# Kernel tuning notes

Hardware: AMD Instinct MI355X
Metric: run time of the kernel (lower is better)

Reference implementation:

```python
import jax, jax.numpy as jnp
import numpy as np
from jax import lax

# ---- model dims ----
NTOKEN = 60697
D_MODEL = 512
NLAYERS = 4
D_STATE = 16
D_CONV = 4
EXPAND = 2
D_INNER = EXPAND * D_MODEL      # 1024
DT_RANK = (D_MODEL + 15) // 16  # 32 (ceil(d_model/16), mamba default)
B_SZ = 4
SEQ = 2048
EPS = 1e-5


def setup_inputs() -> dict:
    key = jax.random.key(0)
    ks = jax.random.split(key, 16)
    s = 0.02
    src = jax.random.randint(ks[0], (B_SZ, SEQ), 0, NTOKEN)
    src_key_padding_mask = jnp.ones((B_SZ, SEQ), dtype=bool)
    emb_w = jax.random.normal(ks[1], (NTOKEN, D_MODEL), jnp.float32) * s
    enc_ln_w = jnp.ones((D_MODEL,), jnp.float32)
    enc_ln_b = jnp.zeros((D_MODEL,), jnp.float32)
    ln_w = jnp.ones((NLAYERS, D_MODEL), jnp.float32)
    ln_b = jnp.zeros((NLAYERS, D_MODEL), jnp.float32)
    in_proj_w = jax.random.normal(ks[2], (NLAYERS, 2 * D_INNER, D_MODEL), jnp.float32) * s
    conv_w = jax.random.normal(ks[3], (NLAYERS, D_INNER, D_CONV), jnp.float32) * 0.1
    conv_b = jnp.zeros((NLAYERS, D_INNER), jnp.float32)
    x_proj_w = jax.random.normal(ks[4], (NLAYERS, DT_RANK + 2 * D_STATE, D_INNER), jnp.float32) * s
    dt_proj_w = jax.random.normal(ks[5], (NLAYERS, D_INNER, DT_RANK), jnp.float32) * (DT_RANK ** -0.5)
    dt_proj_b = jax.random.uniform(ks[6], (NLAYERS, D_INNER), jnp.float32, -4.0, -2.0)
    # S4D real init: A = -[1..d_state], stored as log
    A_log = jnp.log(jnp.broadcast_to(jnp.arange(1, D_STATE + 1, dtype=jnp.float32),
                                     (NLAYERS, D_INNER, D_STATE)))
    D_skip = jnp.ones((NLAYERS, D_INNER), jnp.float32)
    out_proj_w = jax.random.normal(ks[7], (NLAYERS, D_MODEL, D_INNER), jnp.float32) * s / np.sqrt(NLAYERS)
    normf_w = jnp.ones((D_MODEL,), jnp.float32)
    normf_b = jnp.zeros((D_MODEL,), jnp.float32)
    return {
        'src': src, 'src_key_padding_mask': src_key_padding_mask,
        'emb_w': emb_w, 'enc_ln_w': enc_ln_w, 'enc_ln_b': enc_ln_b,
        'ln_w': ln_w, 'ln_b': ln_b, 'in_proj_w': in_proj_w,
        'conv_w': conv_w, 'conv_b': conv_b, 'x_proj_w': x_proj_w,
        'dt_proj_w': dt_proj_w, 'dt_proj_b': dt_proj_b,
        'A_log': A_log, 'D_skip': D_skip, 'out_proj_w': out_proj_w,
        'normf_w': normf_w, 'normf_b': normf_b,
    }


def _layer_norm(x, w, b, eps=EPS):
    mu = jnp.mean(x, axis=-1, keepdims=True)
    var = jnp.mean(jnp.square(x - mu), axis=-1, keepdims=True)
    return (x - mu) * lax.rsqrt(var + eps) * w + b


def _mamba_mixer(h, in_w, cw, cb, xw, dtw, dtb, A_log, D_skip, ow):
    B, L, _ = h.shape
    xz = h @ in_w.T                                   # [B,L,2*d_inner]
    x, z = jnp.split(xz, 2, axis=-1)
    # causal depthwise conv1d, kernel D_CONV
    xt = x.swapaxes(1, 2)                             # [B,d_inner,L]
    xp = jnp.pad(xt, ((0, 0), (0, 0), (D_CONV - 1, 0)))
    conv = cb[None, :, None]
    for k in range(D_CONV):
        conv = conv + cw[:, k][None, :, None] * xp[:, :, k:k + L]
    x = jax.nn.silu(conv).swapaxes(1, 2)              # [B,L,d_inner]
    xdbl = x @ xw.T                                   # [B,L,dt_rank+2*d_state]
    dt = jax.nn.softplus(xdbl[..., :DT_RANK] @ dtw.T + dtb)      # [B,L,d_inner]
    Bm = xdbl[..., DT_RANK:DT_RANK + D_STATE]                    # [B,L,d_state]
    Cm = xdbl[..., DT_RANK + D_STATE:]                           # [B,L,d_state]
    A = -jnp.exp(A_log)                               # [d_inner,d_state]

    def step(hst, inp):
        dt_t, b_t, c_t, x_t = inp                     # [B,d_inner],[B,d_state],[B,d_state],[B,d_inner]
        dA = jnp.exp(dt_t[..., None] * A)             # [B,d_inner,d_state]
        hst = dA * hst + (dt_t * x_t)[..., None] * b_t[:, None, :]
        y_t = jnp.einsum('bds,bs->bd', hst, c_t)
        return hst, y_t

    xs = (dt.swapaxes(0, 1), Bm.swapaxes(0, 1), Cm.swapaxes(0, 1), x.swapaxes(0, 1))
    h0 = jnp.zeros((B, D_INNER, D_STATE), dtype=h.dtype)
    _, ys = lax.scan(step, h0, xs)                    # ys: [L,B,d_inner]
    y = ys.swapaxes(0, 1) + x * D_skip
    y = y * jax.nn.silu(z)
    return y @ ow.T


def reference(src, src_key_padding_mask, emb_w, enc_ln_w, enc_ln_b, ln_w, ln_b,
              in_proj_w, conv_w, conv_b, x_proj_w, dt_proj_w, dt_proj_b,
              A_log, D_skip, out_proj_w, normf_w, normf_b):
    # GeneEncoder: embedding -> LayerNorm (dropout = identity in eval)
    hidden = _layer_norm(emb_w[src], enc_ln_w, enc_ln_b)
    residual = None
    for i in range(NLAYERS):  # prenorm Mamba Blocks
        residual = hidden if residual is None else hidden + residual
        hidden = _mamba_mixer(_layer_norm(residual, ln_w[i], ln_b[i]),
                              in_proj_w[i], conv_w[i], conv_b[i], x_proj_w[i],
                              dt_proj_w[i], dt_proj_b[i], A_log[i], D_skip[i],
                              out_proj_w[i])
    residual = hidden + residual
    return _layer_norm(residual, normf_w, normf_b)
```

## Files before the change

### kernel.cpp

```cpp
#include <hip/hip_runtime.h>
#include <hip/hip_bf16.h>
#include <math.h>

#define NTOKEN 60697
#define D_MODEL 512
#define NLAYERS 4
#define D_STATE 16
#define D_CONV 4
#define D_INNER 1024
#define DT_RANK 32
#define B_SZ 4
#define SEQ 2048
#define EPS 1e-5f
#define NROWS (B_SZ * SEQ)
#define CHUNK 128
#define NCHUNK (SEQ / CHUNK)

typedef __bf16 bf16_t;
typedef __attribute__((ext_vector_type(8))) __bf16 bfx8;
typedef __attribute__((ext_vector_type(4))) __bf16 bfx4;
typedef __attribute__((ext_vector_type(4))) float f32x4;


__device__ __forceinline__ float fast_sigmoid(float x) {
    return 1.0f / (1.0f + __expf(-x));
}
__device__ __forceinline__ float silu(float x) {
    return x * fast_sigmoid(x);
}
__device__ __forceinline__ float softplus_f(float x) {
    return (x > 20.0f) ? x : log1pf(__expf(x));
}

__device__ __forceinline__ void gload_lds16(const void* g, void* l) {
    __builtin_amdgcn_global_load_lds(
        (const __attribute__((address_space(1))) unsigned int*)g,
        (__attribute__((address_space(3))) unsigned int*)l, 16, 0, 0);
}

template <int CTRL>
__device__ __forceinline__ float dpp_fetch(float x) {
    int xi = __builtin_bit_cast(int, x);
    int yi = __builtin_amdgcn_update_dpp(0, xi, CTRL, 0xF, 0xF, true);
    return __builtin_bit_cast(float, yi);
}
__device__ __forceinline__ float dpp_sum16(float p) {
    p += dpp_fetch<0xB1>(p);
    p += dpp_fetch<0x4E>(p);
    p += dpp_fetch<0x141>(p);
    p += dpp_fetch<0x140>(p);
    return p;
}

__device__ __forceinline__ float blk_reduce_sum(float x, float* sbuf) {
#pragma unroll
    for (int m = 32; m >= 1; m >>= 1) x += __shfl_xor(x, m);
    int wid = threadIdx.x >> 6;
    if ((threadIdx.x & 63) == 0) sbuf[wid] = x;
    __syncthreads();
    float t = sbuf[0] + sbuf[1] + sbuf[2] + sbuf[3];
    __syncthreads();
    return t;
}

__global__ __launch_bounds__(256) void cast_bf16_kernel(
    const float* __restrict__ in, bf16_t* __restrict__ out, size_t n)
{
    size_t stride = (size_t)gridDim.x * 256 * 4;
    for (size_t i = ((size_t)blockIdx.x * 256 + threadIdx.x) * 4; i < n; i += stride) {
        float4 v = *reinterpret_cast<const float4*>(in + i);
        bfx4 o;
        o[0] = (bf16_t)v.x; o[1] = (bf16_t)v.y;
        o[2] = (bf16_t)v.z; o[3] = (bf16_t)v.w;
        *reinterpret_cast<bfx4*>(out + i) = o;
    }
}

__global__ __launch_bounds__(256) void weff_kernel(
    const float* __restrict__ dtw, const float* __restrict__ xw,
    bf16_t* __restrict__ Weff)
{
    int L = blockIdx.y;
    int idx = blockIdx.x * 256 + threadIdx.x;
    int n = idx >> 10, k = idx & 1023;
    const float* dtwL = dtw + (size_t)L * D_INNER * DT_RANK;
    const float* xwL  = xw  + (size_t)L * (DT_RANK + 2 * D_STATE) * D_INNER;
    float acc = 0.f;
#pragma unroll
    for (int r = 0; r < DT_RANK; r++)
        acc += dtwL[n * DT_RANK + r] * xwL[r * D_INNER + k];
    Weff[(size_t)L * D_INNER * D_INNER + idx] = (bf16_t)acc;
}


__global__ __launch_bounds__(256) void embed_ln_kernel(
    const int* __restrict__ src, const float* __restrict__ emb,
    const float* __restrict__ w, const float* __restrict__ b,
    float* __restrict__ R)
{
    __shared__ float sbuf[4];
    int row = blockIdx.x;
    int tok = src[row];
    const float* e = emb + (size_t)tok * D_MODEL;
    int c0 = threadIdx.x, c1 = threadIdx.x + 256;
    float v0 = e[c0], v1 = e[c1];
    float mu = blk_reduce_sum(v0 + v1, sbuf) * (1.0f / D_MODEL);
    float d0 = v0 - mu, d1 = v1 - mu;
    float var = blk_reduce_sum(d0 * d0 + d1 * d1, sbuf) * (1.0f / D_MODEL);
    float rs = rsqrtf(var + EPS);
    size_t base = (size_t)row * D_MODEL;
    R[base + c0] = d0 * rs * w[c0] + b[c0];
    R[base + c1] = d1 * rs * w[c1] + b[c1];
}

__global__ __launch_bounds__(256) void add_ln_kernel(
    float* __restrict__ R, const float* __restrict__ Hadd,
    const float* __restrict__ w, const float* __restrict__ b,
    float* __restrict__ out, bf16_t* __restrict__ outb)
{
    __shared__ float sbuf[4];
    size_t base = (size_t)blockIdx.x * D_MODEL;
    int c0 = threadIdx.x, c1 = c0 + 256;
    float v0 = R[base + c0], v1 = R[base + c1];
    if (Hadd) {
        v0 += Hadd[base + c0];
        v1 += Hadd[base + c1];
        R[base + c0] = v0;
        R[base + c1] = v1;
    }
    float mu = blk_reduce_sum(v0 + v1, sbuf) * (1.0f / D_MODEL);
    float d0 = v0 - mu, d1 = v1 - mu;
    float var = blk_reduce_sum(d0 * d0 + d1 * d1, sbuf) * (1.0f / D_MODEL);
    float rs = rsqrtf(var + EPS);
    float o0 = d0 * rs * w[c0] + b[c0];
    float o1 = d1 * rs * w[c1] + b[c1];
    if (out) {
        out[base + c0] = o0;
        out[base + c1] = o1;
    }
    if (outb) {
        outb[base + c0] = (bf16_t)o0;
        outb[base + c1] = (bf16_t)o1;
    }
}

template <int EPI>
__global__ __launch_bounds__(256) void gemm_bf16_nt(
    const bf16_t* __restrict__ A, const bf16_t* __restrict__ B,
    float* __restrict__ C, int ldc, int K, const float* __restrict__ bias,
    const unsigned short* __restrict__ xcb_u16,
    unsigned short* __restrict__ dtx_u16,
    float* __restrict__ Cz)
{
    __shared__ bf16_t As[128 * 32];
    __shared__ bf16_t Bs[128 * 32];
    int tid = threadIdx.x;
    int lane = tid & 63, wid = tid >> 6;
    int m0 = blockIdx.y * 128, n0 = blockIdx.x * 128;
    int wm = (wid >> 1) * 64, wn = (wid & 1) * 64;
    int c_lo = lane & 15;
    int khalf = lane >> 4;

    f32x4 acc[4][4];
#pragma unroll
    for (int i = 0; i < 4; i++)
#pragma unroll
        for (int j = 0; j < 4; j++)
            acc[i][j] = (f32x4){0.f, 0.f, 0.f, 0.f};

    for (int k0 = 0; k0 < K; k0 += 32) {
#pragma unroll
        for (int i = 0; i < 2; i++) {
            int c = i * 256 + tid;
            int row = c >> 2;
            int cb = (c & 3) * 16;
            int ldsoff = (i * 256 + wid * 64) * 16;
            gload_lds16((const char*)A + ((size_t)(m0 + row) * K + k0) * 2 + cb,
                        (char*)As + ldsoff);
            gload_lds16((const char*)B + ((size_t)(n0 + row) * K + k0) * 2 + cb,
                        (char*)Bs + ldsoff);
        }
        __syncthreads();

        bfx8 af[4], bfr[4];
#pragma unroll
        for (int i = 0; i < 4; i++) {
            af[i]  = *reinterpret_cast<const bfx8*>(As + (wm + i * 16 + c_lo) * 32 + khalf * 8);
            bfr[i] = *reinterpret_cast<const bfx8*>(Bs + (wn + i * 16 + c_lo) * 32 + khalf * 8);
        }
#pragma unroll
        for (int i = 0; i < 4; i++)
#pragma unroll
            for (int j = 0; j < 4; j++)
                acc[i][j] = __builtin_amdgcn_mfma_f32_16x16x32_bf16(af[i], bfr[j], acc[i][j], 0, 0, 0);
        __syncthreads();
    }

#pragma unroll
    for (int i = 0; i < 4; i++) {
#pragma unroll
        for (int j = 0; j < 4; j++) {
            int row0 = m0 + wm + i * 16 + khalf * 4;
            int col = n0 + wn + j * 16 + c_lo;
#pragma unroll
            for (int r = 0; r < 4; r++) {
                int row = row0 + r;
                float v = acc[i][j][r];
                if (EPI == 0) {
                    C[(size_t)row * ldc + col] = v;
                } else if (EPI == 2) {
                    v = softplus_f(v + bias[col]);
                    unsigned int db = (unsigned int)__builtin_bit_cast(unsigned short, (bf16_t)v);
                    unsigned int xb = (unsigned int)xcb_u16[(size_t)row * D_INNER + col];
                    *(unsigned int*)(dtx_u16 + (size_t)row * 2048 + 2 * col) = db | (xb << 16);
                } else if (EPI == 3) {
                    if (col < D_INNER) C[(size_t)row * D_INNER + col] = v;
                    else               Cz[(size_t)row * D_INNER + col - D_INNER] = v;
                }
            }
        }
    }
}

__global__ __launch_bounds__(128) void gemm_bc_bf16(
    const bf16_t* __restrict__ A, const bf16_t* __restrict__ Bmat,
    float* __restrict__ BCX, int K)
{
    __shared__ bf16_t As[64 * 32];
    __shared__ bf16_t Bs[32 * 32];
    int tid = threadIdx.x;
    int lane = tid & 63, w = tid >> 6;
    int m0 = blockIdx.x * 64;
    int wr0 = w * 32;
    int c_lo = lane & 15;
    int khalf = lane >> 4;

    f32x4 acc[2][2];
#pragma unroll
    for (int i = 0; i < 2; i++)
#pragma unroll
        for (int j = 0; j < 2; j++)
            acc[i][j] = (f32x4){0.f, 0.f, 0.f, 0.f};

    for (int k0 = 0; k0 < K; k0 += 32) {
        {
            int c = tid;
            gload_lds16((const char*)A + ((size_t)(m0 + (c >> 2)) * K + k0) * 2 + (c & 3) * 16,
                        (char*)As + w * 1024);
        }
        {
            int c = tid + 128;
            gload_lds16((const char*)A + ((size_t)(m0 + (c >> 2)) * K + k0) * 2 + (c & 3) * 16,
                        (char*)As + 2048 + w * 1024);
        }
        {
            int c = tid;
            gload_lds16((const char*)Bmat + ((size_t)(c >> 2) * K + k0) * 2 + (c & 3) * 16,
                        (char*)Bs + w * 1024);
        }
        __syncthreads();

        bfx8 af[2], bfr[2];
#pragma unroll
        for (int i = 0; i < 2; i++)
            af[i] = *reinterpret_cast<const bfx8*>(As + (wr0 + i * 16 + c_lo) * 32 + khalf * 8);
#pragma unroll
        for (int j = 0; j < 2; j++)
            bfr[j] = *reinterpret_cast<const bfx8*>(Bs + (j * 16 + c_lo) * 32 + khalf * 8);
#pragma unroll
        for (int i = 0; i < 2; i++)
#pragma unroll
            for (int j = 0; j < 2; j++)
                acc[i][j] = __builtin_amdgcn_mfma_f32_16x16x32_bf16(af[i], bfr[j], acc[i][j], 0, 0, 0);
        __syncthreads();
    }

#pragma unroll
    for (int i = 0; i < 2; i++)
#pragma unroll
        for (int j = 0; j < 2; j++) {
            int row0 = m0 + wr0 + i * 16 + khalf * 4;
#pragma unroll
            for (int r = 0; r < 4; r++)
                BCX[(size_t)(row0 + r) * 32 + 2 * c_lo + j] = acc[i][j][r];
        }
}

__global__ __launch_bounds__(256) void conv_silu_kernel(
    const float* __restrict__ Xraw, const float* __restrict__ cw,
    const float* __restrict__ cb, bf16_t* __restrict__ XCb)
{
    size_t gid = (size_t)blockIdx.x * 256 + threadIdx.x;
    int d = (int)(gid & (D_INNER - 1));
    size_t bt = gid >> 10;
    int t = (int)(bt & (SEQ - 1));
    float acc = cb[d];
#pragma unroll
    for (int k = 0; k < D_CONV; k++) {
        int tt = t + k - (D_CONV - 1);
        if (tt >= 0)
            acc += cw[d * D_CONV + k] * Xraw[(bt + (size_t)(k - (D_CONV - 1))) * D_INNER + d];
    }
    XCb[gid] = (bf16_t)silu(acc);
}

__device__ __forceinline__ void scan_stage(
    char* base, const unsigned int* __restrict__ DTXb,
    const float* __restrict__ BCX, size_t r0, int d0, int w, int lane)
{
    if (w < 2) {
        int cdt = w * 64 + lane;
        gload_lds16((const char*)DTXb + ((r0 + (cdt >> 2)) * 1024 + d0) * 4 + (cdt & 3) * 16,
                    base + w * 1024);
        int cbc = 128 + w * 64;
        gload_lds16((const char*)BCX + (r0 + ((cbc + lane) >> 3)) * 128 + ((cbc + lane) & 7) * 16,
                    base + 2048 + cbc * 16);
    } else {
        int cbc = (w - 2) * 64;
        gload_lds16((const char*)BCX + (r0 + ((cbc + lane) >> 3)) * 128 + ((cbc + lane) & 7) * 16,
                    base + 2048 + cbc * 16);
    }
}

__global__ __launch_bounds__(256) void scan_pA_kernel(
    const unsigned int* __restrict__ DTXb, const float* __restrict__ BCX,
    const float* __restrict__ A_log,
    float* __restrict__ DcB, float* __restrict__ UcB)
{
    __shared__ __align__(16) char lds[2][6144];
    const int tid = threadIdx.x;
    const int w = tid >> 6, lane = tid & 63;
    const int s = tid & 15, dl = tid >> 4;
    const int b = blockIdx.x >> 6;
    const int d0 = (blockIdx.x & 63) * 16;
    const int c = blockIdx.y;
    const int d = d0 + dl;
    const float Av = -__expf(A_log[d * D_STATE + s]);
    const size_t bbase = (size_t)b * SEQ;
    const int tstart = c * CHUNK;

    float h = 0.f, cum = 0.f;
    scan_stage(lds[0], DTXb, BCX, bbase + tstart, d0, w, lane);
    __syncthreads();
    int cur = 0;
    for (int t0 = 0; t0 < CHUNK; t0 += 32) {
        if (t0 + 32 < CHUNK)
            scan_stage(lds[cur ^ 1], DTXb, BCX, bbase + tstart + t0 + 32, d0, w, lane);
        const char* L = lds[cur];
#pragma unroll
        for (int kk = 0; kk < 32; kk++) {
            unsigned int pk = *(const unsigned int*)(L + kk * 64 + dl * 4);
            float dtv = __builtin_bit_cast(float, pk << 16);
            float xv  = __builtin_bit_cast(float, pk & 0xFFFF0000u);
            float bv  = *(const float*)(L + 2048 + kk * 128 + s * 8);
            float e = __expf(dtv * Av);
            h = fmaf(e, h, dtv * xv * bv);
            cum += dtv;
        }
        __syncthreads();
        cur ^= 1;
    }
    size_t cb64 = ((size_t)c * B_SZ + b) * D_INNER + d;
    UcB[cb64 * 16 + s] = h;
    if (s == 0) DcB[cb64] = cum;
}

__global__ __launch_bounds__(256) void scan_p2_kernel(
    const float* __restrict__ A_log, const float* __restrict__ DcB,
    const float* __restrict__ UcB, float* __restrict__ HcB)
{
    int tid = threadIdx.x;
    int s = tid & 15, dl = tid >> 4;
    int chain = blockIdx.x * 16 + dl;
    int b = chain >> 10, d = chain & 1023;
    float Av = -__expf(A_log[d * D_STATE + s]);
    float Hv = 0.f;
    for (int c = 0; c < NCHUNK; c++) {
        size_t base = ((size_t)c * B_SZ + b) * D_INNER + d;
        HcB[base * 16 + s] = Hv;
        Hv = __expf(Av * DcB[base]) * Hv + UcB[base * 16 + s];
    }
}

__global__ __launch_bounds__(256) void scan_pB_kernel(
    const unsigned int* __restrict__ DTXb, const float* __restrict__ BCX,
    const float* __restrict__ HcB, const float* __restrict__ A_log,
    const float* __restrict__ Zbuf, const float* __restrict__ Dskip,
    bf16_t* __restrict__ XCb)
{
    __shared__ __align__(16) char lds[2][6144];
    __shared__ float ytile[32][17];
    const int tid = threadIdx.x;
    const int w = tid >> 6, lane = tid & 63;
    const int s = tid & 15, dl = tid >> 4;
    const int b = blockIdx.x >> 6;
    const int d0 = (blockIdx.x & 63) * 16;
    const int c = blockIdx.y;
    const int d = d0 + dl;
    const float Av = -__expf(A_log[d * D_STATE + s]);
    const size_t bbase = (size_t)b * SEQ;
    const int tstart = c * CHUNK;

    float h = HcB[(((size_t)c * B_SZ + b) * D_INNER + d) * 16 + s];

    const int tl  = tid >> 3;
    const int dlo = (tid * 2) & 15;
    const float dsk0 = Dskip[d0 + dlo];
    const float dsk1 = Dskip[d0 + dlo + 1];

    scan_stage(lds[0], DTXb, BCX, bbase + tstart, d0, w, lane);
    __syncthreads();
    int cur = 0;
    for (int t0 = 0; t0 < CHUNK; t0 += 32) {
        if (t0 + 32 < CHUNK)
            scan_stage(lds[cur ^ 1], DTXb, BCX, bbase + tstart + t0 + 32, d0, w, lane);
        const char* L = lds[cur];
#pragma unroll
        for (int half = 0; half < 2; half++) {
            float yhold = 0.f;
#pragma unroll
            for (int k = 0; k < 16; k++) {
                int kk = half * 16 + k;
                unsigned int pk = *(const unsigned int*)(L + kk * 64 + dl * 4);
                float dtv = __builtin_bit_cast(float, pk << 16);
                float xv  = __builtin_bit_cast(float, pk & 0xFFFF0000u);
                float2 bc = *(const float2*)(L + 2048 + kk * 128 + s * 8);
                float e = __expf(dtv * Av);
                h = fmaf(e, h, dtv * xv * bc.x);
                float p = dpp_sum16(h * bc.y);
                if (s == k) yhold = p;
            }
            ytile[half * 16 + s][dl] = yhold;
        }
        __syncthreads();

        {
            int t = tstart + t0 + tl;
            size_t row = (bbase + t) * (size_t)D_INNER + d0 + dlo;
            float y0 = ytile[tl][dlo];
            float y1 = ytile[tl][dlo + 1];
            unsigned int xw = *(const unsigned int*)(XCb + row);
            float x0 = __builtin_bit_cast(float, xw << 16);
            float x1 = __builtin_bit_cast(float, xw & 0xFFFF0000u);
            float2 z2 = *(const float2*)(Zbuf + row);
            float g0 = (y0 + x0 * dsk0) * silu(z2.x);
            float g1 = (y1 + x1 * dsk1) * silu(z2.y);
            unsigned int o = (unsigned int)__builtin_bit_cast(unsigned short, (bf16_t)g0)
                           | ((unsigned int)__builtin_bit_cast(unsigned short, (bf16_t)g1) << 16);
            *(unsigned int*)(XCb + row) = o;
        }
        __syncthreads();
        cur ^= 1;
    }
}


extern "C" void kernel_launch(void* const* d_in, const int* in_sizes, int n_in,
                              void* d_out, int out_size, void* d_ws, size_t ws_size,
                              hipStream_t stream) {
    const int*   src       = (const int*)d_in[0];
    const float* emb_w     = (const float*)d_in[2];
    const float* enc_ln_w  = (const float*)d_in[3];
    const float* enc_ln_b  = (const float*)d_in[4];
    const float* ln_w      = (const float*)d_in[5];
    const float* ln_b      = (const float*)d_in[6];
    const float* in_proj_w = (const float*)d_in[7];
    const float* conv_w    = (const float*)d_in[8];
    const float* conv_b    = (const float*)d_in[9];
    const float* x_proj_w  = (const float*)d_in[10];
    const float* dt_proj_w = (const float*)d_in[11];
    const float* dt_proj_b = (const float*)d_in[12];
    const float* A_log     = (const float*)d_in[13];
    const float* D_skip    = (const float*)d_in[14];
    const float* out_proj_w= (const float*)d_in[15];
    const float* normf_w   = (const float*)d_in[16];
    const float* normf_b   = (const float*)d_in[17];
    float* out = (float*)d_out;

    float* R    = (float*)d_ws;
    float* H    = R    + (size_t)NROWS * D_MODEL;
    float* Xraw = H    + (size_t)NROWS * D_MODEL;
    float* Zbuf = Xraw + (size_t)NROWS * D_INNER;
    float* BCX  = Zbuf + (size_t)NROWS * D_INNER;
    float* DcB  = BCX  + (size_t)NROWS * 32;
    float* UcB  = DcB  + (size_t)NCHUNK * B_SZ * D_INNER;
    float* HcB  = UcB  + (size_t)NCHUNK * B_SZ * D_INNER * D_STATE;
    bf16_t* Hb   = (bf16_t*)(HcB + (size_t)NCHUNK * B_SZ * D_INNER * D_STATE);
    bf16_t* XCb  = Hb  + (size_t)NROWS * D_MODEL;
    unsigned short* DTXb = (unsigned short*)(XCb + (size_t)NROWS * D_INNER);
    bf16_t* Wib   = (bf16_t*)(DTXb + (size_t)NROWS * 2048);
    bf16_t* Wob   = Wib   + (size_t)NLAYERS * 2 * D_INNER * D_MODEL;
    bf16_t* Weffb = Wob   + (size_t)NLAYERS * D_MODEL * D_INNER;
    bf16_t* xpb   = Weffb + (size_t)NLAYERS * D_INNER * D_INNER;

    cast_bf16_kernel<<<2048, 256, 0, stream>>>(in_proj_w, Wib, (size_t)NLAYERS * 2 * D_INNER * D_MODEL);
    cast_bf16_kernel<<<2048, 256, 0, stream>>>(out_proj_w, Wob, (size_t)NLAYERS * D_MODEL * D_INNER);
    cast_bf16_kernel<<<256, 256, 0, stream>>>(x_proj_w, xpb, (size_t)NLAYERS * (DT_RANK + 2 * D_STATE) * D_INNER);
    weff_kernel<<<dim3(4096, NLAYERS), 256, 0, stream>>>(dt_proj_w, x_proj_w, Weffb);

    embed_ln_kernel<<<NROWS, 256, 0, stream>>>(src, emb_w, enc_ln_w, enc_ln_b, R);

    for (int L = 0; L < NLAYERS; L++) {
        const float* AlogL = A_log + (size_t)L * D_INNER * D_STATE;

        add_ln_kernel<<<NROWS, 256, 0, stream>>>(
            R, (L == 0) ? nullptr : H, ln_w + L * D_MODEL, ln_b + L * D_MODEL,
            nullptr, Hb);

        gemm_bf16_nt<3><<<dim3(16, 64), 256, 0, stream>>>(
            Hb, Wib + (size_t)L * 2 * D_INNER * D_MODEL, Xraw, D_INNER, D_MODEL,
            nullptr, nullptr, nullptr, Zbuf);

        conv_silu_kernel<<<(NROWS * D_INNER) / 256, 256, 0, stream>>>(
            Xraw, conv_w + (size_t)L * D_INNER * D_CONV, conv_b + (size_t)L * D_INNER, XCb);

        gemm_bc_bf16<<<NROWS / 64, 128, 0, stream>>>(
            XCb, xpb + (size_t)L * 64 * D_INNER + (size_t)DT_RANK * D_INNER, BCX, D_INNER);

        gemm_bf16_nt<2><<<dim3(8, 64), 256, 0, stream>>>(
            XCb, Weffb + (size_t)L * D_INNER * D_INNER, nullptr, 0, D_INNER,
            dt_proj_b + (size_t)L * D_INNER, (const unsigned short*)XCb, DTXb, nullptr);

        scan_pA_kernel<<<dim3(B_SZ * 64, NCHUNK), 256, 0, stream>>>(
            (const unsigned int*)DTXb, BCX, AlogL, DcB, UcB);
        scan_p2_kernel<<<256, 256, 0, stream>>>(AlogL, DcB, UcB, HcB);
        scan_pB_kernel<<<dim3(B_SZ * 64, NCHUNK), 256, 0, stream>>>(
            (const unsigned int*)DTXb, BCX, HcB, AlogL, Zbuf,
            D_skip + (size_t)L * D_INNER, XCb);

        gemm_bf16_nt<0><<<dim3(4, 64), 256, 0, stream>>>(
            XCb, Wob + (size_t)L * D_MODEL * D_INNER, H, D_MODEL, D_INNER,
            nullptr, nullptr, nullptr, nullptr);
    }

    add_ln_kernel<<<NROWS, 256, 0, stream>>>(R, H, normf_w, normf_b, out, nullptr);
}
```

Measured before the change: 1.214 ms.

## Replace fused dt weight with low-rank path and store in_proj outputs in bf16

Removes the precomputed 1024x1024 effective dt weight. The x_proj GEMM now produces the 32-wide low-rank dt projection as bf16 alongside B and C, and dt_proj runs as a K=32 GEMM, which cuts the dt GEMM FLOPs and weight traffic by a large factor. Separately, the x and z outputs of in_proj are written as bf16 instead of fp32, halving that memory traffic in conv and scan. This adds an extra rounding of the intermediate activations and a dependency between the two small GEMMs.

```diff
diff --git a/kernel.cpp b/kernel.cpp
--- a/kernel.cpp
+++ b/kernel.cpp
@@ -76,22 +76,6 @@
     }
 }
 
-__global__ __launch_bounds__(256) void weff_kernel(
-    const float* __restrict__ dtw, const float* __restrict__ xw,
-    bf16_t* __restrict__ Weff)
-{
-    int L = blockIdx.y;
-    int idx = blockIdx.x * 256 + threadIdx.x;
-    int n = idx >> 10, k = idx & 1023;
-    const float* dtwL = dtw + (size_t)L * D_INNER * DT_RANK;
-    const float* xwL  = xw  + (size_t)L * (DT_RANK + 2 * D_STATE) * D_INNER;
-    float acc = 0.f;
-#pragma unroll
-    for (int r = 0; r < DT_RANK; r++)
-        acc += dtwL[n * DT_RANK + r] * xwL[r * D_INNER + k];
-    Weff[(size_t)L * D_INNER * D_INNER + idx] = (bf16_t)acc;
-}
-
 
 __global__ __launch_bounds__(256) void embed_ln_kernel(
     const int* __restrict__ src, const float* __restrict__ emb,
@@ -150,7 +134,7 @@
     float* __restrict__ C, int ldc, int K, const float* __restrict__ bias,
     const unsigned short* __restrict__ xcb_u16,
     unsigned short* __restrict__ dtx_u16,
-    float* __restrict__ Cz)
+    bf16_t* __restrict__ Cxb, bf16_t* __restrict__ Czb)
 {
     __shared__ bf16_t As[128 * 32];
     __shared__ bf16_t Bs[128 * 32];
@@ -214,20 +198,20 @@
                     unsigned int xb = (unsigned int)xcb_u16[(size_t)row * D_INNER + col];
                     *(unsigned int*)(dtx_u16 + (size_t)row * 2048 + 2 * col) = db | (xb << 16);
                 } else if (EPI == 3) {
-                    if (col < D_INNER) C[(size_t)row * D_INNER + col] = v;
-                    else               Cz[(size_t)row * D_INNER + col - D_INNER] = v;
+                    if (col < D_INNER) Cxb[(size_t)row * D_INNER + col] = (bf16_t)v;
+                    else               Czb[(size_t)row * D_INNER + col - D_INNER] = (bf16_t)v;
                 }
             }
         }
     }
 }
 
-__global__ __launch_bounds__(128) void gemm_bc_bf16(
+__global__ __launch_bounds__(128) void gemm_xp_bf16(
     const bf16_t* __restrict__ A, const bf16_t* __restrict__ Bmat,
-    float* __restrict__ BCX, int K)
+    bf16_t* __restrict__ XDlow, float* __restrict__ BCX, int K)
 {
     __shared__ bf16_t As[64 * 32];
-    __shared__ bf16_t Bs[32 * 32];
+    __shared__ bf16_t Bs[64 * 32];
     int tid = threadIdx.x;
     int lane = tid & 63, w = tid >> 6;
     int m0 = blockIdx.x * 64;
@@ -235,42 +219,36 @@
     int c_lo = lane & 15;
     int khalf = lane >> 4;
 
-    f32x4 acc[2][2];
+    f32x4 acc[2][4];
 #pragma unroll
     for (int i = 0; i < 2; i++)
 #pragma unroll
-        for (int j = 0; j < 2; j++)
+        for (int j = 0; j < 4; j++)
             acc[i][j] = (f32x4){0.f, 0.f, 0.f, 0.f};
 
     for (int k0 = 0; k0 < K; k0 += 32) {
-        {
-            int c = tid;
+#pragma unroll
+        for (int call = 0; call < 2; call++) {
+            int c = call * 128 + tid;
+            int base = (call * 128 + w * 64) * 16;
             gload_lds16((const char*)A + ((size_t)(m0 + (c >> 2)) * K + k0) * 2 + (c & 3) * 16,
-                        (char*)As + w * 1024);
-        }
-        {
-            int c = tid + 128;
-            gload_lds16((const char*)A + ((size_t)(m0 + (c >> 2)) * K + k0) * 2 + (c & 3) * 16,
-                        (char*)As + 2048 + w * 1024);
-        }
-        {
-            int c = tid;
+                        (char*)As + base);
             gload_lds16((const char*)Bmat + ((size_t)(c >> 2) * K + k0) * 2 + (c & 3) * 16,
-                        (char*)Bs + w * 1024);
-        }
-        __syncthreads();
-
-        bfx8 af[2], bfr[2];
+                        (char*)Bs + base);
+        }
+        __syncthreads();
+
+        bfx8 af[2], bfr[4];
 #pragma unroll
         for (int i = 0; i < 2; i++)
             af[i] = *reinterpret_cast<const bfx8*>(As + (wr0 + i * 16 + c_lo) * 32 + khalf * 8);
 #pragma unroll
-        for (int j = 0; j < 2; j++)
+        for (int j = 0; j < 4; j++)
             bfr[j] = *reinterpret_cast<const bfx8*>(Bs + (j * 16 + c_lo) * 32 + khalf * 8);
 #pragma unroll
         for (int i = 0; i < 2; i++)
 #pragma unroll
-            for (int j = 0; j < 2; j++)
+            for (int j = 0; j < 4; j++)
                 acc[i][j] = __builtin_amdgcn_mfma_f32_16x16x32_bf16(af[i], bfr[j], acc[i][j], 0, 0, 0);
         __syncthreads();
     }
@@ -278,16 +256,25 @@
 #pragma unroll
     for (int i = 0; i < 2; i++)
 #pragma unroll
-        for (int j = 0; j < 2; j++) {
+        for (int j = 0; j < 4; j++) {
             int row0 = m0 + wr0 + i * 16 + khalf * 4;
-#pragma unroll
-            for (int r = 0; r < 4; r++)
-                BCX[(size_t)(row0 + r) * 32 + 2 * c_lo + j] = acc[i][j][r];
+            int col = j * 16 + c_lo;
+#pragma unroll
+            for (int r = 0; r < 4; r++) {
+                int row = row0 + r;
+                float v = acc[i][j][r];
+                if (col < DT_RANK) {
+                    XDlow[(size_t)row * DT_RANK + col] = (bf16_t)v;
+                } else {
+                    int c2 = col - DT_RANK;
+                    BCX[(size_t)row * 32 + 2 * (c2 & 15) + (c2 >> 4)] = v;
+                }
+            }
         }
 }
 
 __global__ __launch_bounds__(256) void conv_silu_kernel(
-    const float* __restrict__ Xraw, const float* __restrict__ cw,
+    const bf16_t* __restrict__ Xrawb, const float* __restrict__ cw,
     const float* __restrict__ cb, bf16_t* __restrict__ XCb)
 {
     size_t gid = (size_t)blockIdx.x * 256 + threadIdx.x;
@@ -299,7 +286,7 @@
     for (int k = 0; k < D_CONV; k++) {
         int tt = t + k - (D_CONV - 1);
         if (tt >= 0)
-            acc += cw[d * D_CONV + k] * Xraw[(bt + (size_t)(k - (D_CONV - 1))) * D_INNER + d];
+            acc += cw[d * D_CONV + k] * (float)Xrawb[(bt + (size_t)(k - (D_CONV - 1))) * D_INNER + d];
     }
     XCb[gid] = (bf16_t)silu(acc);
 }
@@ -385,7 +372,7 @@
 __global__ __launch_bounds__(256) void scan_pB_kernel(
     const unsigned int* __restrict__ DTXb, const float* __restrict__ BCX,
     const float* __restrict__ HcB, const float* __restrict__ A_log,
-    const float* __restrict__ Zbuf, const float* __restrict__ Dskip,
+    const bf16_t* __restrict__ Zbufb, const float* __restrict__ Dskip,
     bf16_t* __restrict__ XCb)
 {
     __shared__ __align__(16) char lds[2][6144];
@@ -442,9 +429,11 @@
             unsigned int xw = *(const unsigned int*)(XCb + row);
             float x0 = __builtin_bit_cast(float, xw << 16);
             float x1 = __builtin_bit_cast(float, xw & 0xFFFF0000u);
-            float2 z2 = *(const float2*)(Zbuf + row);
-            float g0 = (y0 + x0 * dsk0) * silu(z2.x);
-            float g1 = (y1 + x1 * dsk1) * silu(z2.y);
+            unsigned int zw = *(const unsigned int*)(Zbufb + row);
+            float z0 = __builtin_bit_cast(float, zw << 16);
+            float z1 = __builtin_bit_cast(float, zw & 0xFFFF0000u);
+            float g0 = (y0 + x0 * dsk0) * silu(z0);
+            float g1 = (y1 + x1 * dsk1) * silu(z1);
             unsigned int o = (unsigned int)__builtin_bit_cast(unsigned short, (bf16_t)g0)
                            | ((unsigned int)__builtin_bit_cast(unsigned short, (bf16_t)g1) << 16);
             *(unsigned int*)(XCb + row) = o;
@@ -479,24 +468,25 @@
 
     float* R    = (float*)d_ws;
     float* H    = R    + (size_t)NROWS * D_MODEL;
-    float* Xraw = H    + (size_t)NROWS * D_MODEL;
-    float* Zbuf = Xraw + (size_t)NROWS * D_INNER;
-    float* BCX  = Zbuf + (size_t)NROWS * D_INNER;
+    float* BCX  = H    + (size_t)NROWS * D_MODEL;
     float* DcB  = BCX  + (size_t)NROWS * 32;
     float* UcB  = DcB  + (size_t)NCHUNK * B_SZ * D_INNER;
     float* HcB  = UcB  + (size_t)NCHUNK * B_SZ * D_INNER * D_STATE;
-    bf16_t* Hb   = (bf16_t*)(HcB + (size_t)NCHUNK * B_SZ * D_INNER * D_STATE);
-    bf16_t* XCb  = Hb  + (size_t)NROWS * D_MODEL;
-    unsigned short* DTXb = (unsigned short*)(XCb + (size_t)NROWS * D_INNER);
+    bf16_t* Hb    = (bf16_t*)(HcB + (size_t)NCHUNK * B_SZ * D_INNER * D_STATE);
+    bf16_t* Xrawb = Hb    + (size_t)NROWS * D_MODEL;
+    bf16_t* Zbufb = Xrawb + (size_t)NROWS * D_INNER;
+    bf16_t* XCb   = Zbufb + (size_t)NROWS * D_INNER;
+    bf16_t* XDlow = XCb   + (size_t)NROWS * D_INNER;
+    unsigned short* DTXb = (unsigned short*)(XDlow + (size_t)NROWS * DT_RANK);
     bf16_t* Wib   = (bf16_t*)(DTXb + (size_t)NROWS * 2048);
     bf16_t* Wob   = Wib   + (size_t)NLAYERS * 2 * D_INNER * D_MODEL;
-    bf16_t* Weffb = Wob   + (size_t)NLAYERS * D_MODEL * D_INNER;
-    bf16_t* xpb   = Weffb + (size_t)NLAYERS * D_INNER * D_INNER;
+    bf16_t* xpb   = Wob   + (size_t)NLAYERS * D_MODEL * D_INNER;
+    bf16_t* dtwb  = xpb   + (size_t)NLAYERS * 64 * D_INNER;
 
     cast_bf16_kernel<<<2048, 256, 0, stream>>>(in_proj_w, Wib, (size_t)NLAYERS * 2 * D_INNER * D_MODEL);
     cast_bf16_kernel<<<2048, 256, 0, stream>>>(out_proj_w, Wob, (size_t)NLAYERS * D_MODEL * D_INNER);
-    cast_bf16_kernel<<<256, 256, 0, stream>>>(x_proj_w, xpb, (size_t)NLAYERS * (DT_RANK + 2 * D_STATE) * D_INNER);
-    weff_kernel<<<dim3(4096, NLAYERS), 256, 0, stream>>>(dt_proj_w, x_proj_w, Weffb);
+    cast_bf16_kernel<<<256, 256, 0, stream>>>(x_proj_w, xpb, (size_t)NLAYERS * 64 * D_INNER);
+    cast_bf16_kernel<<<128, 256, 0, stream>>>(dt_proj_w, dtwb, (size_t)NLAYERS * D_INNER * DT_RANK);
 
     embed_ln_kernel<<<NROWS, 256, 0, stream>>>(src, emb_w, enc_ln_w, enc_ln_b, R);
 
@@ -508,29 +498,30 @@
             nullptr, Hb);
 
         gemm_bf16_nt<3><<<dim3(16, 64), 256, 0, stream>>>(
-            Hb, Wib + (size_t)L * 2 * D_INNER * D_MODEL, Xraw, D_INNER, D_MODEL,
-            nullptr, nullptr, nullptr, Zbuf);
+            Hb, Wib + (size_t)L * 2 * D_INNER * D_MODEL, nullptr, 0, D_MODEL,
+            nullptr, nullptr, nullptr, Xrawb, Zbufb);
 
         conv_silu_kernel<<<(NROWS * D_INNER) / 256, 256, 0, stream>>>(
-            Xraw, conv_w + (size_t)L * D_INNER * D_CONV, conv_b + (size_t)L * D_INNER, XCb);
-
-        gemm_bc_bf16<<<NROWS / 64, 128, 0, stream>>>(
-            XCb, xpb + (size_t)L * 64 * D_INNER + (size_t)DT_RANK * D_INNER, BCX, D_INNER);
+            Xrawb, conv_w + (size_t)L * D_INNER * D_CONV, conv_b + (size_t)L * D_INNER, XCb);
+
+        gemm_xp_bf16<<<NROWS / 64, 128, 0, stream>>>(
+            XCb, xpb + (size_t)L * 64 * D_INNER, XDlow, BCX, D_INNER);
 
         gemm_bf16_nt<2><<<dim3(8, 64), 256, 0, stream>>>(
-            XCb, Weffb + (size_t)L * D_INNER * D_INNER, nullptr, 0, D_INNER,
-            dt_proj_b + (size_t)L * D_INNER, (const unsigned short*)XCb, DTXb, nullptr);
+            XDlow, dtwb + (size_t)L * D_INNER * DT_RANK, nullptr, 0, DT_RANK,
+            dt_proj_b + (size_t)L * D_INNER, (const unsigned short*)XCb, DTXb,
+            nullptr, nullptr);
 
         scan_pA_kernel<<<dim3(B_SZ * 64, NCHUNK), 256, 0, stream>>>(
             (const unsigned int*)DTXb, BCX, AlogL, DcB, UcB);
         scan_p2_kernel<<<256, 256, 0, stream>>>(AlogL, DcB, UcB, HcB);
         scan_pB_kernel<<<dim3(B_SZ * 64, NCHUNK), 256, 0, stream>>>(
-            (const unsigned int*)DTXb, BCX, HcB, AlogL, Zbuf,
+            (const unsigned int*)DTXb, BCX, HcB, AlogL, Zbufb,
             D_skip + (size_t)L * D_INNER, XCb);
 
         gemm_bf16_nt<0><<<dim3(4, 64), 256, 0, stream>>>(
             XCb, Wob + (size_t)L * D_MODEL * D_INNER, H, D_MODEL, D_INNER,
-            nullptr, nullptr, nullptr, nullptr);
+            nullptr, nullptr, nullptr, nullptr, nullptr);
     }
 
     add_ln_kernel<<<NROWS, 256, 0, stream>>>(R, H, normf_w, normf_b, out, nullptr);
```

New measurement: 1.091 ms. 1.11x faster.
